# Kernel optimization log

Hardware: AMD Instinct MI355X
Metric: run time of the kernel (lower is better)

Reference implementation:

```python
import jax, jax.numpy as jnp
import numpy as np

B, T, E = 4, 1024, 1024
H, MULT = 16, 2
HD = E // H
SCALE = HD ** -0.5


def setup_inputs() -> dict:
    key = jax.random.key(0)
    ks = jax.random.split(key, 9)
    s = 0.02
    return {
        "hidden_states": jax.random.normal(ks[0], (B, T, E), jnp.float32),
        "attention_mask": jnp.zeros((B, 1, T, T), jnp.float32),
        "Wq": jax.random.normal(ks[1], (E, E), jnp.float32) * s,
        "bq": jnp.zeros((E,), jnp.float32),
        "Wk": jax.random.normal(ks[2], (MULT * E, E), jnp.float32) * s,
        "bk": jnp.zeros((MULT * E,), jnp.float32),
        "Wv": jax.random.normal(ks[3], (MULT * E, E), jnp.float32) * s,
        "bv": jnp.zeros((MULT * E,), jnp.float32),
        "Wo": jax.random.normal(ks[4], (E, E), jnp.float32) * s,
        "bo": jnp.zeros((E,), jnp.float32),
    }


def reference(hidden_states, attention_mask, Wq, bq, Wk, bk, Wv, bv, Wo, bo):
    x = hidden_states  # [B, T, E]
    # q projection, scaled
    q = (jnp.einsum("bte,fe->btf", x, Wq) + bq) * SCALE  # [B,T,E]
    q = q.reshape(B, T, H, HD).transpose(0, 2, 1, 3)      # [B,H,T,HD]
    # k/v project to multiplier-expanded dim, then _shape with seq_len=-1:
    # [B,T,MULT*E] -> view(B, T*MULT, H, HD) (torch view semantics) -> [B,H,T*MULT,HD]
    k = jnp.einsum("bte,fe->btf", x, Wk) + bk             # [B,T,MULT*E]
    k = k.reshape(B, T * MULT, H, HD).transpose(0, 2, 1, 3)
    v = jnp.einsum("bte,fe->btf", x, Wv) + bv
    v = v.reshape(B, T * MULT, H, HD).transpose(0, 2, 1, 3)

    S = T * MULT  # src_len; src_len0 = T
    attn = jnp.einsum("bhtd,bhsd->bhts", q, k)            # [B,H,T,S]
    # custom mask broadcast: view src as [MULT, src_len0] and add mask[:, :, :, None, :]
    attn = attn.reshape(B, H, T, MULT, T) + attention_mask[:, :, :, None, :]
    attn = attn.reshape(B, H, T, S)
    attn = jax.nn.softmax(attn, axis=-1)
    out = jnp.einsum("bhts,bhsd->bhtd", attn, v)          # [B,H,T,HD]
    out = out.transpose(0, 2, 1, 3).reshape(B, T, E)
    out = jnp.einsum("bte,fe->btf", out, Wo) + bo
    return out
```

## Files before the change

### kernel.cpp

```cpp
#include <hip/hip_runtime.h>
#include <math.h>

#define BB    4
#define TT    1024
#define EE    1024
#define HH    16
#define HDIM  64
#define SS    2048
#define MROWS 4096
#define QSCALE 0.18033688011112f
#define LOG2E  1.4426950408889634f

typedef short  s8v  __attribute__((ext_vector_type(8)));
typedef float  f4v  __attribute__((ext_vector_type(4)));

__device__ __forceinline__ unsigned short f2bf(float f) {
    union { float f; unsigned u; } c; c.f = f;
    unsigned u = c.u + 0x7FFFu + ((c.u >> 16) & 1u);
    return (unsigned short)(u >> 16);
}
__device__ __forceinline__ float bflo(unsigned u) {
    union { unsigned u; float f; } c; c.u = u << 16; return c.f;
}
__device__ __forceinline__ float bfhi(unsigned u) {
    union { unsigned u; float f; } c; c.u = u & 0xffff0000u; return c.f;
}

__device__ __forceinline__ void async16(const void* g, void* l) {
    __builtin_amdgcn_global_load_lds(
        (const __attribute__((address_space(1))) unsigned int*)g,
        (__attribute__((address_space(3))) unsigned int*)l,
        16, 0, 0);
}

__global__ __launch_bounds__(256) void cvt6_kernel(
    const float* __restrict__ x,  const float* __restrict__ wq,
    const float* __restrict__ wk, const float* __restrict__ wv,
    const float* __restrict__ wo, const float* __restrict__ mk,
    unsigned short* __restrict__ xb,  unsigned short* __restrict__ wqb,
    unsigned short* __restrict__ wkb, unsigned short* __restrict__ wvb,
    unsigned short* __restrict__ wob, unsigned short* __restrict__ mbb)
{
    const int total = 3670016;
    int i = blockIdx.x * 256 + threadIdx.x;
    const int stride = gridDim.x * 256;
    for (; i < total; i += stride) {
        const float* s; unsigned short* d; int off; float sc = 1.0f;
        if (i < 1048576)      { s = x;  d = xb;  off = i; }
        else if (i < 1310720) { s = wq; d = wqb; off = i - 1048576; }
        else if (i < 1835008) { s = wk; d = wkb; off = i - 1310720; }
        else if (i < 2359296) { s = wv; d = wvb; off = i - 1835008; }
        else if (i < 2621440) { s = wo; d = wob; off = i - 2359296; }
        else                  { s = mk; d = mbb; off = i - 2621440; sc = LOG2E; }
        float4 v = ((const float4*)s)[off];
        ushort4 o;
        o.x = f2bf(v.x * sc); o.y = f2bf(v.y * sc);
        o.z = f2bf(v.z * sc); o.w = f2bf(v.w * sc);
        ((ushort4*)d)[off] = o;
    }
}

#define GEMM_KLOOP(Aptr, Wptr, Ksz)                                            \
    for (int k0 = 0; k0 < (Ksz); k0 += 32) {                                   \
        _Pragma("unroll")                                                      \
        for (int it = 0; it < 2; ++it) {                                       \
            int f = (it * 4 + w) * 64 + lane;                                  \
            int r = f >> 2, g = (f & 3) * 8;                                   \
            async16((Aptr) + (size_t)(m0 + r) * (Ksz) + k0 + g,                \
                    As + (it * 4 + w) * 512);                                  \
            async16((Wptr) + (size_t)(n0 + r) * (Ksz) + k0 + g,                \
                    Bs + (it * 4 + w) * 512);                                  \
        }                                                                      \
        __syncthreads();                                                       \
        s8v af[4], bf[4];                                                      \
        _Pragma("unroll")                                                      \
        for (int i = 0; i < 4; ++i)                                            \
            af[i] = *(const s8v*)(As + (wm + i * 16 + col16) * 32 + quad * 8); \
        _Pragma("unroll")                                                      \
        for (int j = 0; j < 4; ++j)                                            \
            bf[j] = *(const s8v*)(Bs + (wn + j * 16 + col16) * 32 + quad * 8); \
        _Pragma("unroll")                                                      \
        for (int i = 0; i < 4; ++i)                                            \
            _Pragma("unroll")                                                  \
            for (int j = 0; j < 4; ++j)                                        \
                acc[i][j] = __builtin_amdgcn_mfma_f32_16x16x32_bf16(           \
                    af[i], bf[j], acc[i][j], 0, 0, 0);                         \
        __syncthreads();                                                       \
    }

__global__ __launch_bounds__(256, 3) void gemm_qk_kernel(
    const unsigned short* __restrict__ X,  const unsigned short* __restrict__ Wq,
    const unsigned short* __restrict__ Wk, const float* __restrict__ bq,
    const float* __restrict__ bk, unsigned short* __restrict__ qp,
    unsigned short* __restrict__ kp)
{
    __shared__ __align__(16) unsigned short As[128 * 32];
    __shared__ __align__(16) unsigned short Bs[128 * 32];

    const int tid = threadIdx.x;
    const int lane = tid & 63, w = tid >> 6;
    const int wm = (w & 1) * 64, wn = (w >> 1) * 64;
    const int col16 = lane & 15, quad = lane >> 4;
    const int m0 = blockIdx.x * 128;
    const bool isQ = blockIdx.y < 8;
    const int n0 = blockIdx.y * 128;
    const unsigned short* Wrow = isQ ? Wq + (size_t)n0 * EE
                                     : Wk + (size_t)(n0 - EE) * EE;

    f4v acc[4][4];
#pragma unroll
    for (int i = 0; i < 4; ++i)
#pragma unroll
        for (int j = 0; j < 4; ++j) acc[i][j] = (f4v)0.0f;

    for (int k0 = 0; k0 < EE; k0 += 32) {
#pragma unroll
        for (int it = 0; it < 2; ++it) {
            int f = (it * 4 + w) * 64 + lane;
            int r = f >> 2, g = (f & 3) * 8;
            async16(X + (size_t)(m0 + r) * EE + k0 + g, As + (it * 4 + w) * 512);
            async16(Wrow + (size_t)r * EE + k0 + g, Bs + (it * 4 + w) * 512);
        }
        __syncthreads();
        s8v af[4], bf[4];
#pragma unroll
        for (int i = 0; i < 4; ++i)
            af[i] = *(const s8v*)(As + (wm + i * 16 + col16) * 32 + quad * 8);
#pragma unroll
        for (int j = 0; j < 4; ++j)
            bf[j] = *(const s8v*)(Bs + (wn + j * 16 + col16) * 32 + quad * 8);
#pragma unroll
        for (int i = 0; i < 4; ++i)
#pragma unroll
            for (int j = 0; j < 4; ++j)
                acc[i][j] = __builtin_amdgcn_mfma_f32_16x16x32_bf16(
                    af[i], bf[j], acc[i][j], 0, 0, 0);
        __syncthreads();
    }

#pragma unroll
    for (int j = 0; j < 4; ++j) {
        const int n = n0 + wn + j * 16 + col16;
        const float bn = isQ ? bq[n] : bk[n - EE];
#pragma unroll
        for (int i = 0; i < 4; ++i) {
            const int mb = m0 + wm + i * 16 + quad * 4;
#pragma unroll
            for (int r = 0; r < 4; ++r) {
                const int m = mb + r;
                float c = acc[i][j][r] + bn;
                if (isQ) {
                    qp[(size_t)m * EE + n] = f2bf(c * QSCALE);
                } else {
                    const int nk = n - EE;
                    const int mm = nk >> 10, h = (nk >> 6) & 15, d = nk & 63;
                    const int b_ = m >> 10, t = m & 1023;
                    const int s = 2 * t + mm;
                    kp[((size_t)(b_ * HH + h) * SS + s) * HDIM + d] = f2bf(c);
                }
            }
        }
    }
}

template <int LAYOUT, int OUTF32, int Ksz, int Nsz>
__global__ __launch_bounds__(256, 3) void gemm_mfma_kernel(
    const unsigned short* __restrict__ A, const unsigned short* __restrict__ W,
    const float* __restrict__ bias, void* __restrict__ Cout, float alpha)
{
    __shared__ __align__(16) unsigned short As[128 * 32];
    __shared__ __align__(16) unsigned short Bs[128 * 32];

    const int tid = threadIdx.x;
    const int lane = tid & 63, w = tid >> 6;
    const int wm = (w & 1) * 64, wn = (w >> 1) * 64;
    const int col16 = lane & 15, quad = lane >> 4;
    const int m0 = blockIdx.x * 128;
    const int n0 = blockIdx.y * 128;

    f4v acc[4][4];
#pragma unroll
    for (int i = 0; i < 4; ++i)
#pragma unroll
        for (int j = 0; j < 4; ++j) acc[i][j] = (f4v)0.0f;

    GEMM_KLOOP(A, W, Ksz)

#pragma unroll
    for (int j = 0; j < 4; ++j) {
        const int n = n0 + wn + j * 16 + col16;
        const float bn = (LAYOUT == 2) ? 0.0f : bias[n];
#pragma unroll
        for (int i = 0; i < 4; ++i) {
            const int mb = m0 + wm + i * 16 + quad * 4;
#pragma unroll
            for (int r = 0; r < 4; ++r) {
                const int m = mb + r;
                float c = (acc[i][j][r] + ((LAYOUT == 2) ? bias[m] : bn)) * alpha;
                if (LAYOUT == 0) {
                    if (OUTF32) ((float*)Cout)[(size_t)m * Nsz + n] = c;
                    else ((unsigned short*)Cout)[(size_t)m * Nsz + n] = f2bf(c);
                } else {
                    const int mm = m >> 10, h = (m >> 6) & 15, d = m & 63;
                    const int b_ = n >> 10, t = n & 1023;
                    const int s = 2 * t + mm;
                    ((unsigned short*)Cout)[((size_t)(b_ * HH + h) * HDIM + d) * SS + s] = f2bf(c);
                }
            }
        }
    }
}

__global__ __launch_bounds__(256, 4) void attn_mfma5_kernel(
    const unsigned short* __restrict__ Q, const unsigned short* __restrict__ Kh,
    const unsigned short* __restrict__ Vt, const unsigned short* __restrict__ Mb,
    unsigned short* __restrict__ O)
{
    constexpr int PT = 68;
    __shared__ __align__(16) unsigned short K0[64 * PT];
    __shared__ __align__(16) unsigned short K1[64 * PT];
    __shared__ __align__(16) unsigned short V0[64 * PT];
    __shared__ __align__(16) unsigned short V1[64 * PT];

    const int tid = threadIdx.x;
    const int lane = tid & 63, w = tid >> 6;
    const int col16 = lane & 15, quad = lane >> 4;

    const int gid = blockIdx.x;
    const int v = gid & 7, j = gid >> 3;
    const int bh = v * 8 + (j >> 4);
    const int t0 = (j & 15) * 64;
    const int b_ = bh >> 4, h = bh & 15;

    const unsigned short* Qrow =
        Q + (size_t)(b_ * TT + t0 + w * 16 + col16) * EE + h * HDIM;
    const s8v qf0 = *(const s8v*)(Qrow + quad * 8);
    const s8v qf1 = *(const s8v*)(Qrow + 32 + quad * 8);

    f4v oacc[4];
#pragma unroll
    for (int jd = 0; jd < 4; ++jd) oacc[jd] = (f4v)0.0f;
    float mrun = -INFINITY;
    f4v l4 = (f4v)0.0f;

    const unsigned short* Kb   = Kh + (size_t)bh * SS * HDIM;
    const unsigned short* Vb   = Vt + (size_t)bh * HDIM * SS;
    const unsigned short* Mrow = Mb + (size_t)b_ * TT * TT
                               + (size_t)(t0 + w * 16 + col16) * TT;
    const int myrow = (w * 16 + col16) * PT;
    const int r0 = tid >> 3, c0 = (tid & 7) * 8;

    uint4 kA0, kA1, kB0, kB1;
    uint4 vA0, vA1, vB0, vB1;
    uint2 mA0, mA1, mA2, mA3;

#define PREF_K(T2B)                                                            \
    kA0 = *(const uint4*)(Kb + (size_t)((T2B) + r0) * HDIM + c0);              \
    kA1 = *(const uint4*)(Kb + (size_t)((T2B) + r0 + 32) * HDIM + c0);         \
    kB0 = *(const uint4*)(Kb + (size_t)(1024 + (T2B) + r0) * HDIM + c0);       \
    kB1 = *(const uint4*)(Kb + (size_t)(1024 + (T2B) + r0 + 32) * HDIM + c0);
#define PREF_V(T2B)                                                            \
    vA0 = *(const uint4*)(Vb + (size_t)r0 * SS + (T2B) + c0);                  \
    vA1 = *(const uint4*)(Vb + (size_t)(r0 + 32) * SS + (T2B) + c0);           \
    vB0 = *(const uint4*)(Vb + (size_t)r0 * SS + 1024 + (T2B) + c0);           \
    vB1 = *(const uint4*)(Vb + (size_t)(r0 + 32) * SS + 1024 + (T2B) + c0);
#define PREF_M(T2B)                                                            \
    mA0 = *(const uint2*)(Mrow + (T2B) + 0 * 16 + quad * 4);                   \
    mA1 = *(const uint2*)(Mrow + (T2B) + 1 * 16 + quad * 4);                   \
    mA2 = *(const uint2*)(Mrow + (T2B) + 2 * 16 + quad * 4);                   \
    mA3 = *(const uint2*)(Mrow + (T2B) + 3 * 16 + quad * 4);

    PREF_K(0)
    PREF_V(0)
    PREF_M(0)

    for (int it16 = 0; it16 < 16; ++it16) {
        __syncthreads();

        *(uint4*)(K0 + r0 * PT + c0)        = kA0;
        *(uint4*)(K0 + (r0 + 32) * PT + c0) = kA1;
        *(uint4*)(K1 + r0 * PT + c0)        = kB0;
        *(uint4*)(K1 + (r0 + 32) * PT + c0) = kB1;
        *(uint4*)(V0 + r0 * PT + c0)        = vA0;
        *(uint4*)(V0 + (r0 + 32) * PT + c0) = vA1;
        *(uint4*)(V1 + r0 * PT + c0)        = vB0;
        *(uint4*)(V1 + (r0 + 32) * PT + c0) = vB1;

        f4v s0acc[4], s1acc[4];
        {
            f4v mv;
            mv[0] = bflo(mA0.x); mv[1] = bfhi(mA0.x);
            mv[2] = bflo(mA0.y); mv[3] = bfhi(mA0.y);
            s0acc[0] = mv; s1acc[0] = mv;
            mv[0] = bflo(mA1.x); mv[1] = bfhi(mA1.x);
            mv[2] = bflo(mA1.y); mv[3] = bfhi(mA1.y);
            s0acc[1] = mv; s1acc[1] = mv;
            mv[0] = bflo(mA2.x); mv[1] = bfhi(mA2.x);
            mv[2] = bflo(mA2.y); mv[3] = bfhi(mA2.y);
            s0acc[2] = mv; s1acc[2] = mv;
            mv[0] = bflo(mA3.x); mv[1] = bfhi(mA3.x);
            mv[2] = bflo(mA3.y); mv[3] = bfhi(mA3.y);
            s0acc[3] = mv; s1acc[3] = mv;
        }

        const int t2n = ((it16 + 1) & 15) * 64;
        PREF_K(t2n)
        PREF_M(t2n)

        __syncthreads();

        __builtin_amdgcn_s_setprio(1);
#pragma unroll
        for (int ks = 0; ks < 2; ++ks) {
            const s8v bq_ = ks ? qf1 : qf0;
#pragma unroll
            for (int js = 0; js < 4; ++js) {
                s8v ak0 = *(const s8v*)(K0 + (js * 16 + col16) * PT + ks * 32 + quad * 8);
                s8v ak1 = *(const s8v*)(K1 + (js * 16 + col16) * PT + ks * 32 + quad * 8);
                s0acc[js] = __builtin_amdgcn_mfma_f32_16x16x32_bf16(ak0, bq_, s0acc[js], 0, 0, 0);
                s1acc[js] = __builtin_amdgcn_mfma_f32_16x16x32_bf16(ak1, bq_, s1acc[js], 0, 0, 0);
            }
        }
        __builtin_amdgcn_s_setprio(0);

        float tm0 = fmaxf(fmaxf(s0acc[0][0], s0acc[0][1]), fmaxf(s0acc[0][2], s0acc[0][3]));
        float tm1 = fmaxf(fmaxf(s0acc[1][0], s0acc[1][1]), fmaxf(s0acc[1][2], s0acc[1][3]));
        float tm2 = fmaxf(fmaxf(s0acc[2][0], s0acc[2][1]), fmaxf(s0acc[2][2], s0acc[2][3]));
        float tm3 = fmaxf(fmaxf(s0acc[3][0], s0acc[3][1]), fmaxf(s0acc[3][2], s0acc[3][3]));
        float tn0 = fmaxf(fmaxf(s1acc[0][0], s1acc[0][1]), fmaxf(s1acc[0][2], s1acc[0][3]));
        float tn1 = fmaxf(fmaxf(s1acc[1][0], s1acc[1][1]), fmaxf(s1acc[1][2], s1acc[1][3]));
        float tn2 = fmaxf(fmaxf(s1acc[2][0], s1acc[2][1]), fmaxf(s1acc[2][2], s1acc[2][3]));
        float tn3 = fmaxf(fmaxf(s1acc[3][0], s1acc[3][1]), fmaxf(s1acc[3][2], s1acc[3][3]));
        float tmax = fmaxf(fmaxf(fmaxf(tm0, tm1), fmaxf(tm2, tm3)),
                           fmaxf(fmaxf(tn0, tn1), fmaxf(tn2, tn3)));

        if (!__all(tmax - mrun <= 10.0f)) {
            float tfull = fmaxf(tmax, __shfl_xor(tmax, 16));
            tfull = fmaxf(tfull, __shfl_xor(tfull, 32));
            const float mnew = fmaxf(mrun, tfull);
            const float scl = __builtin_amdgcn_exp2f(mrun - mnew);
            l4 *= scl;
            float sclr[4];
#pragma unroll
            for (int r = 0; r < 4; ++r) sclr[r] = __shfl(scl, quad * 4 + r);
#pragma unroll
            for (int jd = 0; jd < 4; ++jd)
#pragma unroll
                for (int r = 0; r < 4; ++r) oacc[jd][r] *= sclr[r];
            mrun = mnew;
        }

        unsigned pk0[8], pk1[8];
#pragma unroll
        for (int js = 0; js < 4; ++js) {
            f4v p0 = s0acc[js] - mrun;
            f4v p1 = s1acc[js] - mrun;
#pragma unroll
            for (int r = 0; r < 4; ++r) {
                p0[r] = __builtin_amdgcn_exp2f(p0[r]);
                p1[r] = __builtin_amdgcn_exp2f(p1[r]);
            }
            l4 += p0 + p1;
            __asm__("v_cvt_pk_bf16_f32 %0, %1, %2" : "=v"(pk0[js*2])   : "v"(p0[0]), "v"(p0[1]));
            __asm__("v_cvt_pk_bf16_f32 %0, %1, %2" : "=v"(pk0[js*2+1]) : "v"(p0[2]), "v"(p0[3]));
            __asm__("v_cvt_pk_bf16_f32 %0, %1, %2" : "=v"(pk1[js*2])   : "v"(p1[0]), "v"(p1[1]));
            __asm__("v_cvt_pk_bf16_f32 %0, %1, %2" : "=v"(pk1[js*2+1]) : "v"(p1[2]), "v"(p1[3]));
        }

        PREF_V(t2n)

        __syncthreads();

#pragma unroll
        for (int js = 0; js < 4; ++js) {
            *(uint2*)(K0 + myrow + js * 16 + quad * 4) = make_uint2(pk0[js*2], pk0[js*2+1]);
            *(uint2*)(K1 + myrow + js * 16 + quad * 4) = make_uint2(pk1[js*2], pk1[js*2+1]);
        }

        __builtin_amdgcn_s_setprio(1);
#pragma unroll
        for (int ks = 0; ks < 2; ++ks) {
            s8v p0 = *(const s8v*)(K0 + myrow + ks * 32 + quad * 8);
            s8v p1 = *(const s8v*)(K1 + myrow + ks * 32 + quad * 8);
#pragma unroll
            for (int jd = 0; jd < 4; ++jd) {
                s8v v0_ = *(const s8v*)(V0 + (jd * 16 + col16) * PT + ks * 32 + quad * 8);
                s8v v1_ = *(const s8v*)(V1 + (jd * 16 + col16) * PT + ks * 32 + quad * 8);
                oacc[jd] = __builtin_amdgcn_mfma_f32_16x16x32_bf16(p0, v0_, oacc[jd], 0, 0, 0);
                oacc[jd] = __builtin_amdgcn_mfma_f32_16x16x32_bf16(p1, v1_, oacc[jd], 0, 0, 0);
            }
        }
        __builtin_amdgcn_s_setprio(0);
    }
#undef PREF_K
#undef PREF_V
#undef PREF_M

    float lr = l4[0] + l4[1] + l4[2] + l4[3];
    lr += __shfl_xor(lr, 16);
    lr += __shfl_xor(lr, 32);
    const float inv = 1.0f / lr;
    float invr[4];
#pragma unroll
    for (int r = 0; r < 4; ++r) invr[r] = __shfl(inv, quad * 4 + r);
#pragma unroll
    for (int r = 0; r < 4; ++r) {
        const int t = t0 + w * 16 + quad * 4 + r;
#pragma unroll
        for (int jd = 0; jd < 4; ++jd)
            O[(size_t)(b_ * TT + t) * EE + h * HDIM + jd * 16 + col16] =
                f2bf(oacc[jd][r] * invr[r]);
    }
}

extern "C" void kernel_launch(void* const* d_in, const int* in_sizes, int n_in,
                              void* d_out, int out_size, void* d_ws, size_t ws_size,
                              hipStream_t stream)
{
    (void)in_sizes; (void)n_in; (void)out_size; (void)ws_size;

    const float* x    = (const float*)d_in[0];
    const float* mask = (const float*)d_in[1];
    const float* Wq   = (const float*)d_in[2];
    const float* bq   = (const float*)d_in[3];
    const float* Wk   = (const float*)d_in[4];
    const float* bk   = (const float*)d_in[5];
    const float* Wv   = (const float*)d_in[6];
    const float* bv   = (const float*)d_in[7];
    const float* Wo   = (const float*)d_in[8];
    const float* bo   = (const float*)d_in[9];
    float* out = (float*)d_out;

    unsigned short* xb  = (unsigned short*)d_ws;
    unsigned short* wqb = xb  + (size_t)MROWS * EE;
    unsigned short* wkb = wqb + (size_t)EE * EE;
    unsigned short* wvb = wkb + (size_t)2 * EE * EE;
    unsigned short* wob = wvb + (size_t)2 * EE * EE;
    unsigned short* mb  = wob + (size_t)EE * EE;
    unsigned short* qp  = mb  + (size_t)BB * TT * TT;
    unsigned short* kp  = qp  + (size_t)MROWS * EE;
    unsigned short* vt  = kp  + (size_t)BB * HH * SS * HDIM;
    unsigned short* ao  = vt  + (size_t)BB * HH * SS * HDIM;

    dim3 blk(256);

    cvt6_kernel<<<4096, blk, 0, stream>>>(x, Wq, Wk, Wv, Wo, mask,
                                          xb, wqb, wkb, wvb, wob, mb);
    gemm_qk_kernel<<<dim3(32, 24), blk, 0, stream>>>(xb, wqb, wkb, bq, bk, qp, kp);
    gemm_mfma_kernel<2, 0, EE, MROWS><<<dim3(16, 32), blk, 0, stream>>>(
        wvb, xb, bv, vt, 1.0f);
    attn_mfma5_kernel<<<dim3(1024), blk, 0, stream>>>(qp, kp, vt, mb, ao);
    gemm_mfma_kernel<0, 1, EE, EE><<<dim3(32, 8), blk, 0, stream>>>(
        ao, wob, bo, out, 1.0f);
}
```

Before: 258.5 us.

## Load V fragments directly from global into registers, drop V LDS staging

The attention kernel no longer stages V tiles through shared memory. Each lane loads its MFMA B-operand fragments straight from the transposed V in global memory, right before the PV matmuls. P is written to separate LDS buffers instead of reusing the K buffers, which removes the second __syncthreads per iteration. This trades LDS traffic and a barrier for redundant per-wave global loads (each of the 4 waves fetches the same V tile) and load latency that is no longer prefetched.

```diff
diff --git a/kernel.cpp b/kernel.cpp
--- a/kernel.cpp
+++ b/kernel.cpp
@@ -211,7 +211,7 @@
     }
 }
 
-__global__ __launch_bounds__(256, 4) void attn_mfma5_kernel(
+__global__ __launch_bounds__(256, 4) void attn_mfma6_kernel(
     const unsigned short* __restrict__ Q, const unsigned short* __restrict__ Kh,
     const unsigned short* __restrict__ Vt, const unsigned short* __restrict__ Mb,
     unsigned short* __restrict__ O)
@@ -219,8 +219,8 @@
     constexpr int PT = 68;
     __shared__ __align__(16) unsigned short K0[64 * PT];
     __shared__ __align__(16) unsigned short K1[64 * PT];
-    __shared__ __align__(16) unsigned short V0[64 * PT];
-    __shared__ __align__(16) unsigned short V1[64 * PT];
+    __shared__ __align__(16) unsigned short P0[64 * PT];
+    __shared__ __align__(16) unsigned short P1[64 * PT];
 
     const int tid = threadIdx.x;
     const int lane = tid & 63, w = tid >> 6;
@@ -249,9 +249,9 @@
                                + (size_t)(t0 + w * 16 + col16) * TT;
     const int myrow = (w * 16 + col16) * PT;
     const int r0 = tid >> 3, c0 = (tid & 7) * 8;
+    const unsigned short* Vlane = Vb + (size_t)col16 * SS + quad * 8;
 
     uint4 kA0, kA1, kB0, kB1;
-    uint4 vA0, vA1, vB0, vB1;
     uint2 mA0, mA1, mA2, mA3;
 
 #define PREF_K(T2B)                                                            \
@@ -259,11 +259,6 @@
     kA1 = *(const uint4*)(Kb + (size_t)((T2B) + r0 + 32) * HDIM + c0);         \
     kB0 = *(const uint4*)(Kb + (size_t)(1024 + (T2B) + r0) * HDIM + c0);       \
     kB1 = *(const uint4*)(Kb + (size_t)(1024 + (T2B) + r0 + 32) * HDIM + c0);
-#define PREF_V(T2B)                                                            \
-    vA0 = *(const uint4*)(Vb + (size_t)r0 * SS + (T2B) + c0);                  \
-    vA1 = *(const uint4*)(Vb + (size_t)(r0 + 32) * SS + (T2B) + c0);           \
-    vB0 = *(const uint4*)(Vb + (size_t)r0 * SS + 1024 + (T2B) + c0);           \
-    vB1 = *(const uint4*)(Vb + (size_t)(r0 + 32) * SS + 1024 + (T2B) + c0);
 #define PREF_M(T2B)                                                            \
     mA0 = *(const uint2*)(Mrow + (T2B) + 0 * 16 + quad * 4);                   \
     mA1 = *(const uint2*)(Mrow + (T2B) + 1 * 16 + quad * 4);                   \
@@ -271,20 +266,16 @@
     mA3 = *(const uint2*)(Mrow + (T2B) + 3 * 16 + quad * 4);
 
     PREF_K(0)
-    PREF_V(0)
     PREF_M(0)
 
     for (int it16 = 0; it16 < 16; ++it16) {
+        const int t2b = it16 * 64;
         __syncthreads();
 
         *(uint4*)(K0 + r0 * PT + c0)        = kA0;
         *(uint4*)(K0 + (r0 + 32) * PT + c0) = kA1;
         *(uint4*)(K1 + r0 * PT + c0)        = kB0;
         *(uint4*)(K1 + (r0 + 32) * PT + c0) = kB1;
-        *(uint4*)(V0 + r0 * PT + c0)        = vA0;
-        *(uint4*)(V0 + (r0 + 32) * PT + c0) = vA1;
-        *(uint4*)(V1 + r0 * PT + c0)        = vB0;
-        *(uint4*)(V1 + (r0 + 32) * PT + c0) = vB1;
 
         f4v s0acc[4], s1acc[4];
         {
@@ -367,33 +358,48 @@
             __asm__("v_cvt_pk_bf16_f32 %0, %1, %2" : "=v"(pk1[js*2+1]) : "v"(p1[2]), "v"(p1[3]));
         }
 
-        PREF_V(t2n)
-
-        __syncthreads();
+        __builtin_amdgcn_s_setprio(1);
+
+        s8v vf[8];
+#pragma unroll
+        for (int jd = 0; jd < 4; ++jd)
+#pragma unroll
+            for (int ks = 0; ks < 2; ++ks)
+                vf[jd * 2 + ks] = *(const s8v*)(Vlane + (size_t)(jd * 16) * SS
+                                                + t2b + ks * 32);
 
 #pragma unroll
         for (int js = 0; js < 4; ++js) {
-            *(uint2*)(K0 + myrow + js * 16 + quad * 4) = make_uint2(pk0[js*2], pk0[js*2+1]);
-            *(uint2*)(K1 + myrow + js * 16 + quad * 4) = make_uint2(pk1[js*2], pk1[js*2+1]);
-        }
-
-        __builtin_amdgcn_s_setprio(1);
+            *(uint2*)(P0 + myrow + js * 16 + quad * 4) = make_uint2(pk0[js*2], pk0[js*2+1]);
+            *(uint2*)(P1 + myrow + js * 16 + quad * 4) = make_uint2(pk1[js*2], pk1[js*2+1]);
+        }
+
 #pragma unroll
         for (int ks = 0; ks < 2; ++ks) {
-            s8v p0 = *(const s8v*)(K0 + myrow + ks * 32 + quad * 8);
-            s8v p1 = *(const s8v*)(K1 + myrow + ks * 32 + quad * 8);
-#pragma unroll
-            for (int jd = 0; jd < 4; ++jd) {
-                s8v v0_ = *(const s8v*)(V0 + (jd * 16 + col16) * PT + ks * 32 + quad * 8);
-                s8v v1_ = *(const s8v*)(V1 + (jd * 16 + col16) * PT + ks * 32 + quad * 8);
-                oacc[jd] = __builtin_amdgcn_mfma_f32_16x16x32_bf16(p0, v0_, oacc[jd], 0, 0, 0);
-                oacc[jd] = __builtin_amdgcn_mfma_f32_16x16x32_bf16(p1, v1_, oacc[jd], 0, 0, 0);
-            }
+            s8v p0 = *(const s8v*)(P0 + myrow + ks * 32 + quad * 8);
+#pragma unroll
+            for (int jd = 0; jd < 4; ++jd)
+                oacc[jd] = __builtin_amdgcn_mfma_f32_16x16x32_bf16(
+                    p0, vf[jd * 2 + ks], oacc[jd], 0, 0, 0);
+        }
+
+#pragma unroll
+        for (int jd = 0; jd < 4; ++jd)
+#pragma unroll
+            for (int ks = 0; ks < 2; ++ks)
+                vf[jd * 2 + ks] = *(const s8v*)(Vlane + (size_t)(jd * 16) * SS
+                                                + 1024 + t2b + ks * 32);
+#pragma unroll
+        for (int ks = 0; ks < 2; ++ks) {
+            s8v p1 = *(const s8v*)(P1 + myrow + ks * 32 + quad * 8);
+#pragma unroll
+            for (int jd = 0; jd < 4; ++jd)
+                oacc[jd] = __builtin_amdgcn_mfma_f32_16x16x32_bf16(
+                    p1, vf[jd * 2 + ks], oacc[jd], 0, 0, 0);
         }
         __builtin_amdgcn_s_setprio(0);
     }
 #undef PREF_K
-#undef PREF_V
 #undef PREF_M
 
     float lr = l4[0] + l4[1] + l4[2] + l4[3];
@@ -449,7 +455,7 @@
     gemm_qk_kernel<<<dim3(32, 24), blk, 0, stream>>>(xb, wqb, wkb, bq, bk, qp, kp);
     gemm_mfma_kernel<2, 0, EE, MROWS><<<dim3(16, 32), blk, 0, stream>>>(
         wvb, xb, bv, vt, 1.0f);
-    attn_mfma5_kernel<<<dim3(1024), blk, 0, stream>>>(qp, kp, vt, mb, ao);
+    attn_mfma6_kernel<<<dim3(1024), blk, 0, stream>>>(qp, kp, vt, mb, ao);
     gemm_mfma_kernel<0, 1, EE, EE><<<dim3(32, 8), blk, 0, stream>>>(
         ao, wob, bo, out, 1.0f);
 }
```

Measured after the change: 350.6 us. +35.6%, slower.
